# Performance work log

Hardware: AMD Instinct MI355X
Metric: run time of the kernel (lower is better)

Reference implementation:

```python
import jax, jax.numpy as jnp
import numpy as np

ALPHA = 0.1
DEPTH = 10

N_NODES = 100000
N_EDGES = 3200000
FEATS = 512
HIDDEN = 64
CLASSES = 32


def setup_inputs() -> dict:
    key = jax.random.key(0)
    k1, k2, k3, k4 = jax.random.split(key, 4)
    x = jax.random.normal(k1, (N_NODES, FEATS), dtype=jnp.float32)
    edges = jax.random.randint(k2, (2, N_EDGES), 0, N_NODES, dtype=jnp.int64)
    # Linear weights (stored as [in, out] so forward is x @ W + b)
    W1 = jax.random.normal(k3, (FEATS, HIDDEN), dtype=jnp.float32) * (1.0 / np.sqrt(FEATS))
    b1 = jnp.zeros((HIDDEN,), dtype=jnp.float32)
    W2 = jax.random.normal(k4, (HIDDEN, CLASSES), dtype=jnp.float32) * (1.0 / np.sqrt(HIDDEN))
    b2 = jnp.zeros((CLASSES,), dtype=jnp.float32)
    return {"x": x, "edges": edges, "W1": W1, "b1": b1, "W2": W2, "b2": b2}


def reference(x, edges, W1, b1, W2, b2):
    # Eval mode: all dropouts (feature + edge) are identity.
    n = x.shape[0]
    src, dst = edges[0], edges[1]

    # Symmetric normalization 1/sqrt(deg_src * deg_dst), degrees from in-edges.
    deg = jax.ops.segment_sum(jnp.ones_like(dst, dtype=x.dtype), dst, num_segments=n)
    deg = jnp.maximum(deg, 1.0)
    norm = jax.lax.rsqrt(deg[src] * deg[dst])  # [E]

    # MLP: feats -> hidden -> classes
    h = jax.nn.relu(x @ W1 + b1) @ W2 + b2  # [N, classes]
    h0 = h

    # APPNP propagation: x <- (1-alpha) * A_hat x + alpha * h0
    for _ in range(DEPTH):
        msg = h[src] * norm[:, None]                          # gather  [E, classes]
        agg = jax.ops.segment_sum(msg, dst, num_segments=n)   # scatter [N, classes]
        h = agg * (1.0 - ALPHA) + ALPHA * h0
    return h
```

## Files before the change

### kernel.cpp

```cpp
#include <hip/hip_runtime.h>

#define ALPHA_F 0.1f
#define DEPTH 10
#define FEATS 512
#define HID 64
#define CLS 32

__device__ __forceinline__ unsigned bf16rne(float f) {
  unsigned u = __float_as_uint(f);
  return (u + 0x7fffu + ((u >> 16) & 1u)) >> 16;
}

__global__ __launch_bounds__(256) void k_deg(const int* __restrict__ dst, int E, int N,
                                             unsigned* __restrict__ deg,
                                             unsigned* __restrict__ rank) {
  int i = blockIdx.x * 256 + threadIdx.x;
  if (i >= E) return;
  int d = dst[i];
  unsigned r = 0;
  if ((unsigned)d < (unsigned)N) r = atomicAdd(&deg[d], 1u);
  rank[i] = r;
}

__global__ __launch_bounds__(1024) void k_scan(const unsigned* __restrict__ deg, int N,
                                               unsigned* __restrict__ rowst) {
  __shared__ unsigned sums[1024];
  int t = threadIdx.x;
  int chunk = (N + 1023) >> 10;
  int beg = t * chunk;
  int end = min(beg + chunk, N);
  unsigned s = 0;
  for (int i = beg; i < end; ++i) s += deg[i];
  sums[t] = s;
  __syncthreads();
  for (int off = 1; off < 1024; off <<= 1) {
    unsigned v = (t >= off) ? sums[t - off] : 0u;
    __syncthreads();
    sums[t] += v;
    __syncthreads();
  }
  unsigned pre = (t == 0) ? 0u : sums[t - 1];
  for (int i = beg; i < end; ++i) { rowst[i] = pre; pre += deg[i]; }
  if (t == 1023) rowst[N] = pre;
}

__global__ __launch_bounds__(256) void k_fill(const int* __restrict__ src,
                                              const int* __restrict__ dst,
                                              const unsigned* __restrict__ rank,
                                              const unsigned* __restrict__ rowst,
                                              int E, int N,
                                              int* __restrict__ col) {
  int e = blockIdx.x * 256 + threadIdx.x;
  if (e >= E) return;
  int s = src[e];
  int d = dst[e];
  if ((unsigned)s >= (unsigned)N || (unsigned)d >= (unsigned)N) return;
  col[rowst[d] + rank[e]] = s;
}

__global__ __launch_bounds__(256) void k_mlp(const float* __restrict__ x,
                                             const float* __restrict__ W1,
                                             const float* __restrict__ b1,
                                             const float* __restrict__ W2,
                                             const float* __restrict__ b2,
                                             const unsigned* __restrict__ deg,
                                             float* __restrict__ h0,
                                             unsigned short* __restrict__ u0,
                                             float* __restrict__ rs, int N) {
  __shared__ float XHs[64 * 65];
  __shared__ float W2s[64 * 32];
  __shared__ float b1s[64];
  __shared__ float b2s[32];
  int t = threadIdx.x;
  int m0 = blockIdx.x * 64;

  for (int i = t; i < 64 * 32; i += 256) W2s[i] = W2[i];
  if (t < 64) b1s[t] = b1[t];
  if (t < 32) b2s[t] = b2[t];

  int c = t & 31;
  int h = t >> 5;
  float acc[8][2];
#pragma unroll
  for (int i = 0; i < 8; ++i) { acc[i][0] = 0.f; acc[i][1] = 0.f; }

  for (int k0 = 0; k0 < FEATS; k0 += 64) {
    __syncthreads();
#pragma unroll
    for (int j = 0; j < 2; ++j) {
      int F = j * 256 + t;
      int r = F >> 3, q = F & 7;
      int row = m0 + r;
      float4 v = make_float4(0.f, 0.f, 0.f, 0.f);
      if (row < N) v = *(const float4*)(x + (size_t)row * FEATS + k0 + q * 8);
      *(float4*)(XHs + r * 64 + q * 8) = v;
      float4 v2 = make_float4(0.f, 0.f, 0.f, 0.f);
      if (row < N) v2 = *(const float4*)(x + (size_t)row * FEATS + k0 + q * 8 + 4);
      *(float4*)(XHs + r * 64 + q * 8 + 4) = v2;
    }
    __syncthreads();
    const float* W1p = W1 + (size_t)k0 * 64;
#pragma unroll
    for (int k4 = 0; k4 < 16; ++k4) {
      int k = k4 * 4;
      float4 xv[8];
#pragma unroll
      for (int i = 0; i < 8; ++i) xv[i] = *(const float4*)(XHs + (h * 8 + i) * 64 + k);
#pragma unroll
      for (int j = 0; j < 4; ++j) {
        float w0 = W1p[(k + j) * 64 + c];
        float w1 = W1p[(k + j) * 64 + c + 32];
#pragma unroll
        for (int i = 0; i < 8; ++i) {
          float xx = ((const float*)&xv[i])[j];
          acc[i][0] += xx * w0;
          acc[i][1] += xx * w1;
        }
      }
    }
  }
  __syncthreads();
#pragma unroll
  for (int i = 0; i < 8; ++i) {
    int r = h * 8 + i;
    float v0 = acc[i][0] + b1s[c];
    float v1 = acc[i][1] + b1s[c + 32];
    XHs[r * 65 + c] = v0 > 0.f ? v0 : 0.f;
    XHs[r * 65 + c + 32] = v1 > 0.f ? v1 : 0.f;
  }
  __syncthreads();
  int cc = t & 31;
#pragma unroll
  for (int i = 0; i < 8; ++i) {
    int r = h * 8 + i;
    float s = b2s[cc];
#pragma unroll
    for (int k = 0; k < 64; ++k) s += XHs[r * 65 + k] * W2s[k * 32 + cc];
    int row = m0 + r;
    if (row < N) {
      float dv = (float)deg[row];
      float rsv = rsqrtf(fmaxf(dv, 1.0f));
      h0[(size_t)row * CLS + cc] = s;
      u0[(size_t)row * CLS + cc] = (unsigned short)bf16rne(rsv * s);
      if (cc == 0) rs[row] = rsv;
    }
  }
}

template <bool LAST>
__global__ __launch_bounds__(256) void k_prop(const unsigned* __restrict__ u_in,
                                              const float* __restrict__ h0,
                                              const float* __restrict__ rs,
                                              const unsigned* __restrict__ rowst,
                                              const int* __restrict__ col,
                                              void* __restrict__ out, int N) {
  int t = blockIdx.x * 256 + threadIdx.x;
  int node = t >> 3;
  if (node >= N) return;
  int l = t & 7;
  unsigned beg = rowst[node];
  unsigned end = rowst[node + 1];
  const unsigned* up = u_in + l * 2;
  float a0 = 0.f, a1 = 0.f, a2 = 0.f, a3 = 0.f;
  float b0 = 0.f, b1v = 0.f, b2v = 0.f, b3 = 0.f;
  unsigned e = beg;
  for (; e + 8 <= end; e += 8) {
    int s0 = col[e + 0], s1 = col[e + 1], s2 = col[e + 2], s3 = col[e + 3];
    int s4 = col[e + 4], s5 = col[e + 5], s6 = col[e + 6], s7 = col[e + 7];
    uint2 q0 = *(const uint2*)(up + (size_t)s0 * 16);
    uint2 q1 = *(const uint2*)(up + (size_t)s1 * 16);
    uint2 q2 = *(const uint2*)(up + (size_t)s2 * 16);
    uint2 q3 = *(const uint2*)(up + (size_t)s3 * 16);
    uint2 q4 = *(const uint2*)(up + (size_t)s4 * 16);
    uint2 q5 = *(const uint2*)(up + (size_t)s5 * 16);
    uint2 q6 = *(const uint2*)(up + (size_t)s6 * 16);
    uint2 q7 = *(const uint2*)(up + (size_t)s7 * 16);
    a0 += __uint_as_float(q0.x << 16) + __uint_as_float(q1.x << 16);
    a1 += __uint_as_float(q0.x & 0xffff0000u) + __uint_as_float(q1.x & 0xffff0000u);
    a2 += __uint_as_float(q0.y << 16) + __uint_as_float(q1.y << 16);
    a3 += __uint_as_float(q0.y & 0xffff0000u) + __uint_as_float(q1.y & 0xffff0000u);
    b0 += __uint_as_float(q2.x << 16) + __uint_as_float(q3.x << 16);
    b1v += __uint_as_float(q2.x & 0xffff0000u) + __uint_as_float(q3.x & 0xffff0000u);
    b2v += __uint_as_float(q2.y << 16) + __uint_as_float(q3.y << 16);
    b3 += __uint_as_float(q2.y & 0xffff0000u) + __uint_as_float(q3.y & 0xffff0000u);
    a0 += __uint_as_float(q4.x << 16) + __uint_as_float(q5.x << 16);
    a1 += __uint_as_float(q4.x & 0xffff0000u) + __uint_as_float(q5.x & 0xffff0000u);
    a2 += __uint_as_float(q4.y << 16) + __uint_as_float(q5.y << 16);
    a3 += __uint_as_float(q4.y & 0xffff0000u) + __uint_as_float(q5.y & 0xffff0000u);
    b0 += __uint_as_float(q6.x << 16) + __uint_as_float(q7.x << 16);
    b1v += __uint_as_float(q6.x & 0xffff0000u) + __uint_as_float(q7.x & 0xffff0000u);
    b2v += __uint_as_float(q6.y << 16) + __uint_as_float(q7.y << 16);
    b3 += __uint_as_float(q6.y & 0xffff0000u) + __uint_as_float(q7.y & 0xffff0000u);
  }
  for (; e < end; ++e) {
    int s = col[e];
    uint2 q = *(const uint2*)(up + (size_t)s * 16);
    a0 += __uint_as_float(q.x << 16);
    a1 += __uint_as_float(q.x & 0xffff0000u);
    a2 += __uint_as_float(q.y << 16);
    a3 += __uint_as_float(q.y & 0xffff0000u);
  }
  a0 += b0; a1 += b1v; a2 += b2v; a3 += b3;
  float rsv = rs[node];
  float4 h0v = *(const float4*)(h0 + (size_t)node * CLS + l * 4);
  if (LAST) {
    float ca = ALPHA_F, cb = (1.0f - ALPHA_F) * rsv;
    float4 o = make_float4(ca * h0v.x + cb * a0, ca * h0v.y + cb * a1,
                           ca * h0v.z + cb * a2, ca * h0v.w + cb * a3);
    *(float4*)((float*)out + (size_t)node * CLS + l * 4) = o;
  } else {
    float ca = ALPHA_F * rsv, cb = (1.0f - ALPHA_F) * rsv * rsv;
    float o0 = ca * h0v.x + cb * a0, o1 = ca * h0v.y + cb * a1;
    float o2 = ca * h0v.z + cb * a2, o3 = ca * h0v.w + cb * a3;
    uint2 p;
    p.x = bf16rne(o0) | (bf16rne(o1) << 16);
    p.y = bf16rne(o2) | (bf16rne(o3) << 16);
    *(uint2*)((unsigned*)out + (size_t)node * 16 + l * 2) = p;
  }
}

extern "C" void kernel_launch(void* const* d_in, const int* in_sizes, int n_in,
                              void* d_out, int out_size, void* d_ws, size_t ws_size,
                              hipStream_t stream) {
  const float* x = (const float*)d_in[0];
  const int* edges = (const int*)d_in[1];
  const float* W1 = (const float*)d_in[2];
  const float* b1 = (const float*)d_in[3];
  const float* W2 = (const float*)d_in[4];
  const float* b2 = (const float*)d_in[5];
  int N = in_sizes[0] / FEATS;
  int E = in_sizes[1] / 2;
  const int* src = edges;
  const int* dst = edges + E;

  char* ws = (char*)d_ws;
  auto align64 = [](size_t v) { return (v + 63) & ~(size_t)63; };
  size_t o = 0;
  unsigned* deg = (unsigned*)(ws + o);   o = align64(o + (size_t)N * 4);
  unsigned* rowst = (unsigned*)(ws + o); o = align64(o + (size_t)(N + 1) * 4);
  float* rs = (float*)(ws + o);          o = align64(o + (size_t)N * 4);
  int* col = (int*)(ws + o);             o = align64(o + (size_t)E * 4);
  float* h0 = (float*)(ws + o);          o = align64(o + (size_t)N * CLS * 4);
  unsigned* uA = (unsigned*)(ws + o);    o = align64(o + (size_t)N * CLS * 2);
  unsigned* uB = (unsigned*)(ws + o);    o = align64(o + (size_t)N * CLS * 2);
  unsigned* rank = (unsigned*)h0;

  hipMemsetAsync(deg, 0, (size_t)N * 4, stream);
  k_deg<<<(E + 255) / 256, 256, 0, stream>>>(dst, E, N, deg, rank);
  k_scan<<<1, 1024, 0, stream>>>(deg, N, rowst);
  k_fill<<<(E + 255) / 256, 256, 0, stream>>>(src, dst, rank, rowst, E, N, col);
  k_mlp<<<(N + 63) / 64, 256, 0, stream>>>(x, W1, b1, W2, b2, deg, h0,
                                           (unsigned short*)uA, rs, N);

  float* outF = (float*)d_out;
  const unsigned* uin = uA;
  for (int it = 0; it < DEPTH - 1; ++it) {
    unsigned* uo = (it & 1) ? uA : uB;
    k_prop<false><<<((N * 8) + 255) / 256, 256, 0, stream>>>(uin, h0, rs, rowst, col, uo, N);
    uin = uo;
  }
  k_prop<true><<<((N * 8) + 255) / 256, 256, 0, stream>>>(uin, h0, rs, rowst, col, outF, N);
}
```

Baseline: 1.151 ms.

## Widen MLP tile to 128 rows and use 4 lanes per node in propagation

The MLP kernel now processes 128 rows per block with a 4x8 register tile per thread, loading W1 as float4 and padding the shared tile to stride 68. The point is more register reuse and fewer global W1 loads per FMA. The propagation kernel drops from 8 to 4 lanes per node, each gathering 16 bytes (8 bf16 features) per neighbor instead of 8. That halves the gather instruction count, at the cost of higher register pressure and less thread-level parallelism across the irregular edge lists.

```diff
diff --git a/kernel.cpp b/kernel.cpp
--- a/kernel.cpp
+++ b/kernel.cpp
@@ -10,6 +10,8 @@
   unsigned u = __float_as_uint(f);
   return (u + 0x7fffu + ((u >> 16) & 1u)) >> 16;
 }
+__device__ __forceinline__ float blo(unsigned q) { return __uint_as_float(q << 16); }
+__device__ __forceinline__ float bhi(unsigned q) { return __uint_as_float(q & 0xffff0000u); }
 
 __global__ __launch_bounds__(256) void k_deg(const int* __restrict__ dst, int E, int N,
                                              unsigned* __restrict__ deg,
@@ -67,36 +69,35 @@
                                              float* __restrict__ h0,
                                              unsigned short* __restrict__ u0,
                                              float* __restrict__ rs, int N) {
-  __shared__ float XHs[64 * 65];
+  __shared__ float XHs[128 * 68];
   __shared__ float W2s[64 * 32];
   __shared__ float b1s[64];
   __shared__ float b2s[32];
   int t = threadIdx.x;
-  int m0 = blockIdx.x * 64;
+  int m0 = blockIdx.x * 128;
 
   for (int i = t; i < 64 * 32; i += 256) W2s[i] = W2[i];
   if (t < 64) b1s[t] = b1[t];
   if (t < 32) b2s[t] = b2[t];
 
-  int c = t & 31;
-  int h = t >> 5;
-  float acc[8][2];
-#pragma unroll
-  for (int i = 0; i < 8; ++i) { acc[i][0] = 0.f; acc[i][1] = 0.f; }
+  int c4 = t & 15;
+  int hg = t >> 4;
+  float acc[8][4];
+#pragma unroll
+  for (int i = 0; i < 8; ++i)
+#pragma unroll
+    for (int m = 0; m < 4; ++m) acc[i][m] = 0.f;
 
   for (int k0 = 0; k0 < FEATS; k0 += 64) {
     __syncthreads();
 #pragma unroll
-    for (int j = 0; j < 2; ++j) {
+    for (int j = 0; j < 8; ++j) {
       int F = j * 256 + t;
-      int r = F >> 3, q = F & 7;
+      int r = F >> 4, q = F & 15;
       int row = m0 + r;
       float4 v = make_float4(0.f, 0.f, 0.f, 0.f);
-      if (row < N) v = *(const float4*)(x + (size_t)row * FEATS + k0 + q * 8);
-      *(float4*)(XHs + r * 64 + q * 8) = v;
-      float4 v2 = make_float4(0.f, 0.f, 0.f, 0.f);
-      if (row < N) v2 = *(const float4*)(x + (size_t)row * FEATS + k0 + q * 8 + 4);
-      *(float4*)(XHs + r * 64 + q * 8 + 4) = v2;
+      if (row < N) v = *(const float4*)(x + (size_t)row * FEATS + k0 + q * 4);
+      *(float4*)(XHs + r * 68 + q * 4) = v;
     }
     __syncthreads();
     const float* W1p = W1 + (size_t)k0 * 64;
@@ -105,16 +106,19 @@
       int k = k4 * 4;
       float4 xv[8];
 #pragma unroll
-      for (int i = 0; i < 8; ++i) xv[i] = *(const float4*)(XHs + (h * 8 + i) * 64 + k);
+      for (int i = 0; i < 8; ++i) xv[i] = *(const float4*)(XHs + (i * 16 + hg) * 68 + k);
+      float4 w[4];
+#pragma unroll
+      for (int j = 0; j < 4; ++j) w[j] = *(const float4*)(W1p + (size_t)(k + j) * 64 + c4 * 4);
 #pragma unroll
       for (int j = 0; j < 4; ++j) {
-        float w0 = W1p[(k + j) * 64 + c];
-        float w1 = W1p[(k + j) * 64 + c + 32];
 #pragma unroll
         for (int i = 0; i < 8; ++i) {
           float xx = ((const float*)&xv[i])[j];
-          acc[i][0] += xx * w0;
-          acc[i][1] += xx * w1;
+          acc[i][0] += xx * w[j].x;
+          acc[i][1] += xx * w[j].y;
+          acc[i][2] += xx * w[j].z;
+          acc[i][3] += xx * w[j].w;
         }
       }
     }
@@ -122,20 +126,22 @@
   __syncthreads();
 #pragma unroll
   for (int i = 0; i < 8; ++i) {
-    int r = h * 8 + i;
-    float v0 = acc[i][0] + b1s[c];
-    float v1 = acc[i][1] + b1s[c + 32];
-    XHs[r * 65 + c] = v0 > 0.f ? v0 : 0.f;
-    XHs[r * 65 + c + 32] = v1 > 0.f ? v1 : 0.f;
+    int r = i * 16 + hg;
+    float4 o;
+    o.x = fmaxf(acc[i][0] + b1s[c4 * 4 + 0], 0.f);
+    o.y = fmaxf(acc[i][1] + b1s[c4 * 4 + 1], 0.f);
+    o.z = fmaxf(acc[i][2] + b1s[c4 * 4 + 2], 0.f);
+    o.w = fmaxf(acc[i][3] + b1s[c4 * 4 + 3], 0.f);
+    *(float4*)(XHs + r * 68 + c4 * 4) = o;
   }
   __syncthreads();
-  int cc = t & 31;
-#pragma unroll
-  for (int i = 0; i < 8; ++i) {
-    int r = h * 8 + i;
+  int cc = t & 31, g = t >> 5;
+#pragma unroll
+  for (int i = 0; i < 16; ++i) {
+    int r = i * 8 + g;
     float s = b2s[cc];
 #pragma unroll
-    for (int k = 0; k < 64; ++k) s += XHs[r * 65 + k] * W2s[k * 32 + cc];
+    for (int k = 0; k < 64; ++k) s += XHs[r * 68 + k] * W2s[k * 32 + cc];
     int row = m0 + r;
     if (row < N) {
       float dv = (float)deg[row];
@@ -155,67 +161,75 @@
                                               const int* __restrict__ col,
                                               void* __restrict__ out, int N) {
   int t = blockIdx.x * 256 + threadIdx.x;
-  int node = t >> 3;
+  int node = t >> 2;
   if (node >= N) return;
-  int l = t & 7;
+  int l = t & 3;
   unsigned beg = rowst[node];
   unsigned end = rowst[node + 1];
-  const unsigned* up = u_in + l * 2;
-  float a0 = 0.f, a1 = 0.f, a2 = 0.f, a3 = 0.f;
-  float b0 = 0.f, b1v = 0.f, b2v = 0.f, b3 = 0.f;
+  const uint4* up = (const uint4*)u_in + l;
+  float a[8], b[8];
+#pragma unroll
+  for (int j = 0; j < 8; ++j) { a[j] = 0.f; b[j] = 0.f; }
   unsigned e = beg;
   for (; e + 8 <= end; e += 8) {
     int s0 = col[e + 0], s1 = col[e + 1], s2 = col[e + 2], s3 = col[e + 3];
     int s4 = col[e + 4], s5 = col[e + 5], s6 = col[e + 6], s7 = col[e + 7];
-    uint2 q0 = *(const uint2*)(up + (size_t)s0 * 16);
-    uint2 q1 = *(const uint2*)(up + (size_t)s1 * 16);
-    uint2 q2 = *(const uint2*)(up + (size_t)s2 * 16);
-    uint2 q3 = *(const uint2*)(up + (size_t)s3 * 16);
-    uint2 q4 = *(const uint2*)(up + (size_t)s4 * 16);
-    uint2 q5 = *(const uint2*)(up + (size_t)s5 * 16);
-    uint2 q6 = *(const uint2*)(up + (size_t)s6 * 16);
-    uint2 q7 = *(const uint2*)(up + (size_t)s7 * 16);
-    a0 += __uint_as_float(q0.x << 16) + __uint_as_float(q1.x << 16);
-    a1 += __uint_as_float(q0.x & 0xffff0000u) + __uint_as_float(q1.x & 0xffff0000u);
-    a2 += __uint_as_float(q0.y << 16) + __uint_as_float(q1.y << 16);
-    a3 += __uint_as_float(q0.y & 0xffff0000u) + __uint_as_float(q1.y & 0xffff0000u);
-    b0 += __uint_as_float(q2.x << 16) + __uint_as_float(q3.x << 16);
-    b1v += __uint_as_float(q2.x & 0xffff0000u) + __uint_as_float(q3.x & 0xffff0000u);
-    b2v += __uint_as_float(q2.y << 16) + __uint_as_float(q3.y << 16);
-    b3 += __uint_as_float(q2.y & 0xffff0000u) + __uint_as_float(q3.y & 0xffff0000u);
-    a0 += __uint_as_float(q4.x << 16) + __uint_as_float(q5.x << 16);
-    a1 += __uint_as_float(q4.x & 0xffff0000u) + __uint_as_float(q5.x & 0xffff0000u);
-    a2 += __uint_as_float(q4.y << 16) + __uint_as_float(q5.y << 16);
-    a3 += __uint_as_float(q4.y & 0xffff0000u) + __uint_as_float(q5.y & 0xffff0000u);
-    b0 += __uint_as_float(q6.x << 16) + __uint_as_float(q7.x << 16);
-    b1v += __uint_as_float(q6.x & 0xffff0000u) + __uint_as_float(q7.x & 0xffff0000u);
-    b2v += __uint_as_float(q6.y << 16) + __uint_as_float(q7.y << 16);
-    b3 += __uint_as_float(q6.y & 0xffff0000u) + __uint_as_float(q7.y & 0xffff0000u);
+    uint4 q0 = up[(size_t)s0 * 4];
+    uint4 q1 = up[(size_t)s1 * 4];
+    uint4 q2 = up[(size_t)s2 * 4];
+    uint4 q3 = up[(size_t)s3 * 4];
+    uint4 q4 = up[(size_t)s4 * 4];
+    uint4 q5 = up[(size_t)s5 * 4];
+    uint4 q6 = up[(size_t)s6 * 4];
+    uint4 q7 = up[(size_t)s7 * 4];
+    a[0] += blo(q0.x); a[1] += bhi(q0.x); a[2] += blo(q0.y); a[3] += bhi(q0.y);
+    a[4] += blo(q0.z); a[5] += bhi(q0.z); a[6] += blo(q0.w); a[7] += bhi(q0.w);
+    b[0] += blo(q1.x); b[1] += bhi(q1.x); b[2] += blo(q1.y); b[3] += bhi(q1.y);
+    b[4] += blo(q1.z); b[5] += bhi(q1.z); b[6] += blo(q1.w); b[7] += bhi(q1.w);
+    a[0] += blo(q2.x); a[1] += bhi(q2.x); a[2] += blo(q2.y); a[3] += bhi(q2.y);
+    a[4] += blo(q2.z); a[5] += bhi(q2.z); a[6] += blo(q2.w); a[7] += bhi(q2.w);
+    b[0] += blo(q3.x); b[1] += bhi(q3.x); b[2] += blo(q3.y); b[3] += bhi(q3.y);
+    b[4] += blo(q3.z); b[5] += bhi(q3.z); b[6] += blo(q3.w); b[7] += bhi(q3.w);
+    a[0] += blo(q4.x); a[1] += bhi(q4.x); a[2] += blo(q4.y); a[3] += bhi(q4.y);
+    a[4] += blo(q4.z); a[5] += bhi(q4.z); a[6] += blo(q4.w); a[7] += bhi(q4.w);
+    b[0] += blo(q5.x); b[1] += bhi(q5.x); b[2] += blo(q5.y); b[3] += bhi(q5.y);
+    b[4] += blo(q5.z); b[5] += bhi(q5.z); b[6] += blo(q5.w); b[7] += bhi(q5.w);
+    a[0] += blo(q6.x); a[1] += bhi(q6.x); a[2] += blo(q6.y); a[3] += bhi(q6.y);
+    a[4] += blo(q6.z); a[5] += bhi(q6.z); a[6] += blo(q6.w); a[7] += bhi(q6.w);
+    b[0] += blo(q7.x); b[1] += bhi(q7.x); b[2] += blo(q7.y); b[3] += bhi(q7.y);
+    b[4] += blo(q7.z); b[5] += bhi(q7.z); b[6] += blo(q7.w); b[7] += bhi(q7.w);
   }
   for (; e < end; ++e) {
     int s = col[e];
-    uint2 q = *(const uint2*)(up + (size_t)s * 16);
-    a0 += __uint_as_float(q.x << 16);
-    a1 += __uint_as_float(q.x & 0xffff0000u);
-    a2 += __uint_as_float(q.y << 16);
-    a3 += __uint_as_float(q.y & 0xffff0000u);
-  }
-  a0 += b0; a1 += b1v; a2 += b2v; a3 += b3;
+    uint4 q = up[(size_t)s * 4];
+    a[0] += blo(q.x); a[1] += bhi(q.x); a[2] += blo(q.y); a[3] += bhi(q.y);
+    a[4] += blo(q.z); a[5] += bhi(q.z); a[6] += blo(q.w); a[7] += bhi(q.w);
+  }
+#pragma unroll
+  for (int j = 0; j < 8; ++j) a[j] += b[j];
   float rsv = rs[node];
-  float4 h0v = *(const float4*)(h0 + (size_t)node * CLS + l * 4);
+  const float* h0p = h0 + (size_t)node * CLS + l * 8;
+  float4 h0a = *(const float4*)(h0p);
+  float4 h0b = *(const float4*)(h0p + 4);
   if (LAST) {
     float ca = ALPHA_F, cb = (1.0f - ALPHA_F) * rsv;
-    float4 o = make_float4(ca * h0v.x + cb * a0, ca * h0v.y + cb * a1,
-                           ca * h0v.z + cb * a2, ca * h0v.w + cb * a3);
-    *(float4*)((float*)out + (size_t)node * CLS + l * 4) = o;
+    float* op = (float*)out + (size_t)node * CLS + l * 8;
+    *(float4*)(op) = make_float4(ca * h0a.x + cb * a[0], ca * h0a.y + cb * a[1],
+                                 ca * h0a.z + cb * a[2], ca * h0a.w + cb * a[3]);
+    *(float4*)(op + 4) = make_float4(ca * h0b.x + cb * a[4], ca * h0b.y + cb * a[5],
+                                     ca * h0b.z + cb * a[6], ca * h0b.w + cb * a[7]);
   } else {
     float ca = ALPHA_F * rsv, cb = (1.0f - ALPHA_F) * rsv * rsv;
-    float o0 = ca * h0v.x + cb * a0, o1 = ca * h0v.y + cb * a1;
-    float o2 = ca * h0v.z + cb * a2, o3 = ca * h0v.w + cb * a3;
-    uint2 p;
+    float o0 = ca * h0a.x + cb * a[0], o1 = ca * h0a.y + cb * a[1];
+    float o2 = ca * h0a.z + cb * a[2], o3 = ca * h0a.w + cb * a[3];
+    float o4 = ca * h0b.x + cb * a[4], o5 = ca * h0b.y + cb * a[5];
+    float o6 = ca * h0b.z + cb * a[6], o7 = ca * h0b.w + cb * a[7];
+    uint4 p;
     p.x = bf16rne(o0) | (bf16rne(o1) << 16);
     p.y = bf16rne(o2) | (bf16rne(o3) << 16);
-    *(uint2*)((unsigned*)out + (size_t)node * 16 + l * 2) = p;
+    p.z = bf16rne(o4) | (bf16rne(o5) << 16);
+    p.w = bf16rne(o6) | (bf16rne(o7) << 16);
+    *((uint4*)out + (size_t)node * 4 + l) = p;
   }
 }
 
@@ -249,15 +263,15 @@
   k_deg<<<(E + 255) / 256, 256, 0, stream>>>(dst, E, N, deg, rank);
   k_scan<<<1, 1024, 0, stream>>>(deg, N, rowst);
   k_fill<<<(E + 255) / 256, 256, 0, stream>>>(src, dst, rank, rowst, E, N, col);
-  k_mlp<<<(N + 63) / 64, 256, 0, stream>>>(x, W1, b1, W2, b2, deg, h0,
-                                           (unsigned short*)uA, rs, N);
+  k_mlp<<<(N + 127) / 128, 256, 0, stream>>>(x, W1, b1, W2, b2, deg, h0,
+                                             (unsigned short*)uA, rs, N);
 
   float* outF = (float*)d_out;
   const unsigned* uin = uA;
   for (int it = 0; it < DEPTH - 1; ++it) {
     unsigned* uo = (it & 1) ? uA : uB;
-    k_prop<false><<<((N * 8) + 255) / 256, 256, 0, stream>>>(uin, h0, rs, rowst, col, uo, N);
+    k_prop<false><<<((N * 4) + 255) / 256, 256, 0, stream>>>(uin, h0, rs, rowst, col, uo, N);
     uin = uo;
   }
-  k_prop<true><<<((N * 8) + 255) / 256, 256, 0, stream>>>(uin, h0, rs, rowst, col, outF, N);
-}
+  k_prop<true><<<((N * 4) + 255) / 256, 256, 0, stream>>>(uin, h0, rs, rowst, col, outF, N);
+}
```

After: 1.244 ms. 1.08x slower.

## Pad CSR rows to multiples of 16 with dummy node and widen per-lane gathers

Applied to the files above, without the earlier changes.

Builds a padded CSR in which each row's length is rounded up to a multiple of 16 and the padding slots point to a zeroed dummy node N. The propagation kernel can then drop its remainder loop, read column indices as uint4 vectors and do 16 gathers per iteration. Each node now gets 4 lanes with 16-byte loads instead of 8 lanes with 8-byte loads. h0 is also stored as bf16 to halve that read. The cost is extra padded edge work (up to 15 per node, on average degree 32), an extra col-init kernel, and lower precision in h0.

```diff
diff --git a/kernel.cpp b/kernel.cpp
--- a/kernel.cpp
+++ b/kernel.cpp
@@ -3,13 +3,14 @@
 #define ALPHA_F 0.1f
 #define DEPTH 10
 #define FEATS 512
-#define HID 64
 #define CLS 32
 
 __device__ __forceinline__ unsigned bf16rne(float f) {
   unsigned u = __float_as_uint(f);
   return (u + 0x7fffu + ((u >> 16) & 1u)) >> 16;
 }
+__device__ __forceinline__ float blo(unsigned q) { return __uint_as_float(q << 16); }
+__device__ __forceinline__ float bhi(unsigned q) { return __uint_as_float(q & 0xffff0000u); }
 
 __global__ __launch_bounds__(256) void k_deg(const int* __restrict__ dst, int E, int N,
                                              unsigned* __restrict__ deg,
@@ -22,15 +23,15 @@
   rank[i] = r;
 }
 
-__global__ __launch_bounds__(1024) void k_scan(const unsigned* __restrict__ deg, int N,
-                                               unsigned* __restrict__ rowst) {
+__global__ __launch_bounds__(1024) void k_scanp(const unsigned* __restrict__ deg, int N,
+                                                unsigned* __restrict__ rowst2) {
   __shared__ unsigned sums[1024];
   int t = threadIdx.x;
   int chunk = (N + 1023) >> 10;
   int beg = t * chunk;
   int end = min(beg + chunk, N);
   unsigned s = 0;
-  for (int i = beg; i < end; ++i) s += deg[i];
+  for (int i = beg; i < end; ++i) s += (deg[i] + 15u) & ~15u;
   sums[t] = s;
   __syncthreads();
   for (int off = 1; off < 1024; off <<= 1) {
@@ -40,22 +41,27 @@
     __syncthreads();
   }
   unsigned pre = (t == 0) ? 0u : sums[t - 1];
-  for (int i = beg; i < end; ++i) { rowst[i] = pre; pre += deg[i]; }
-  if (t == 1023) rowst[N] = pre;
+  for (int i = beg; i < end; ++i) { rowst2[i] = pre; pre += (deg[i] + 15u) & ~15u; }
+  if (t == 1023) rowst2[N] = pre;
+}
+
+__global__ __launch_bounds__(256) void k_colinit(unsigned* __restrict__ col2, int cap, int N) {
+  int i = blockIdx.x * 256 + threadIdx.x;
+  if (i < cap) col2[i] = (unsigned)N;
 }
 
 __global__ __launch_bounds__(256) void k_fill(const int* __restrict__ src,
                                               const int* __restrict__ dst,
                                               const unsigned* __restrict__ rank,
-                                              const unsigned* __restrict__ rowst,
+                                              const unsigned* __restrict__ rowst2,
                                               int E, int N,
-                                              int* __restrict__ col) {
+                                              unsigned* __restrict__ col2) {
   int e = blockIdx.x * 256 + threadIdx.x;
   if (e >= E) return;
   int s = src[e];
   int d = dst[e];
   if ((unsigned)s >= (unsigned)N || (unsigned)d >= (unsigned)N) return;
-  col[rowst[d] + rank[e]] = s;
+  col2[rowst2[d] + rank[e]] = (unsigned)s;
 }
 
 __global__ __launch_bounds__(256) void k_mlp(const float* __restrict__ x,
@@ -64,7 +70,7 @@
                                              const float* __restrict__ W2,
                                              const float* __restrict__ b2,
                                              const unsigned* __restrict__ deg,
-                                             float* __restrict__ h0,
+                                             unsigned short* __restrict__ h0b,
                                              unsigned short* __restrict__ u0,
                                              float* __restrict__ rs, int N) {
   __shared__ float XHs[64 * 65];
@@ -140,7 +146,7 @@
     if (row < N) {
       float dv = (float)deg[row];
       float rsv = rsqrtf(fmaxf(dv, 1.0f));
-      h0[(size_t)row * CLS + cc] = s;
+      h0b[(size_t)row * CLS + cc] = (unsigned short)bf16rne(s);
       u0[(size_t)row * CLS + cc] = (unsigned short)bf16rne(rsv * s);
       if (cc == 0) rs[row] = rsv;
     }
@@ -149,73 +155,73 @@
 
 template <bool LAST>
 __global__ __launch_bounds__(256) void k_prop(const unsigned* __restrict__ u_in,
-                                              const float* __restrict__ h0,
+                                              const unsigned short* __restrict__ h0b,
                                               const float* __restrict__ rs,
-                                              const unsigned* __restrict__ rowst,
-                                              const int* __restrict__ col,
+                                              const unsigned* __restrict__ rowst2,
+                                              const unsigned* __restrict__ col2,
                                               void* __restrict__ out, int N) {
   int t = blockIdx.x * 256 + threadIdx.x;
-  int node = t >> 3;
-  if (node >= N) return;
-  int l = t & 7;
-  unsigned beg = rowst[node];
-  unsigned end = rowst[node + 1];
-  const unsigned* up = u_in + l * 2;
-  float a0 = 0.f, a1 = 0.f, a2 = 0.f, a3 = 0.f;
-  float b0 = 0.f, b1v = 0.f, b2v = 0.f, b3 = 0.f;
-  unsigned e = beg;
-  for (; e + 8 <= end; e += 8) {
-    int s0 = col[e + 0], s1 = col[e + 1], s2 = col[e + 2], s3 = col[e + 3];
-    int s4 = col[e + 4], s5 = col[e + 5], s6 = col[e + 6], s7 = col[e + 7];
-    uint2 q0 = *(const uint2*)(up + (size_t)s0 * 16);
-    uint2 q1 = *(const uint2*)(up + (size_t)s1 * 16);
-    uint2 q2 = *(const uint2*)(up + (size_t)s2 * 16);
-    uint2 q3 = *(const uint2*)(up + (size_t)s3 * 16);
-    uint2 q4 = *(const uint2*)(up + (size_t)s4 * 16);
-    uint2 q5 = *(const uint2*)(up + (size_t)s5 * 16);
-    uint2 q6 = *(const uint2*)(up + (size_t)s6 * 16);
-    uint2 q7 = *(const uint2*)(up + (size_t)s7 * 16);
-    a0 += __uint_as_float(q0.x << 16) + __uint_as_float(q1.x << 16);
-    a1 += __uint_as_float(q0.x & 0xffff0000u) + __uint_as_float(q1.x & 0xffff0000u);
-    a2 += __uint_as_float(q0.y << 16) + __uint_as_float(q1.y << 16);
-    a3 += __uint_as_float(q0.y & 0xffff0000u) + __uint_as_float(q1.y & 0xffff0000u);
-    b0 += __uint_as_float(q2.x << 16) + __uint_as_float(q3.x << 16);
-    b1v += __uint_as_float(q2.x & 0xffff0000u) + __uint_as_float(q3.x & 0xffff0000u);
-    b2v += __uint_as_float(q2.y << 16) + __uint_as_float(q3.y << 16);
-    b3 += __uint_as_float(q2.y & 0xffff0000u) + __uint_as_float(q3.y & 0xffff0000u);
-    a0 += __uint_as_float(q4.x << 16) + __uint_as_float(q5.x << 16);
-    a1 += __uint_as_float(q4.x & 0xffff0000u) + __uint_as_float(q5.x & 0xffff0000u);
-    a2 += __uint_as_float(q4.y << 16) + __uint_as_float(q5.y << 16);
-    a3 += __uint_as_float(q4.y & 0xffff0000u) + __uint_as_float(q5.y & 0xffff0000u);
-    b0 += __uint_as_float(q6.x << 16) + __uint_as_float(q7.x << 16);
-    b1v += __uint_as_float(q6.x & 0xffff0000u) + __uint_as_float(q7.x & 0xffff0000u);
-    b2v += __uint_as_float(q6.y << 16) + __uint_as_float(q7.y << 16);
-    b3 += __uint_as_float(q6.y & 0xffff0000u) + __uint_as_float(q7.y & 0xffff0000u);
-  }
-  for (; e < end; ++e) {
-    int s = col[e];
-    uint2 q = *(const uint2*)(up + (size_t)s * 16);
-    a0 += __uint_as_float(q.x << 16);
-    a1 += __uint_as_float(q.x & 0xffff0000u);
-    a2 += __uint_as_float(q.y << 16);
-    a3 += __uint_as_float(q.y & 0xffff0000u);
-  }
-  a0 += b0; a1 += b1v; a2 += b2v; a3 += b3;
-  float rsv = rs[node];
-  float4 h0v = *(const float4*)(h0 + (size_t)node * CLS + l * 4);
+  int g = t >> 2;
+  if (g >= N) return;
+  int l = t & 3;
+  unsigned beg = rowst2[g];
+  unsigned end = rowst2[g + 1];
+  const uint4* up = (const uint4*)u_in + l;
+  const uint4* colv = (const uint4*)col2;
+  float a[8];
+#pragma unroll
+  for (int j = 0; j < 8; ++j) a[j] = 0.f;
+  for (unsigned e = beg; e < end; e += 16) {
+    unsigned e4 = e >> 2;
+    uint4 c0 = colv[e4 + 0];
+    uint4 c1 = colv[e4 + 1];
+    uint4 c2 = colv[e4 + 2];
+    uint4 c3 = colv[e4 + 3];
+    uint4 q0 = up[(size_t)c0.x * 4];
+    uint4 q1 = up[(size_t)c0.y * 4];
+    uint4 q2 = up[(size_t)c0.z * 4];
+    uint4 q3 = up[(size_t)c0.w * 4];
+    uint4 q4 = up[(size_t)c1.x * 4];
+    uint4 q5 = up[(size_t)c1.y * 4];
+    uint4 q6 = up[(size_t)c1.z * 4];
+    uint4 q7 = up[(size_t)c1.w * 4];
+    uint4 q8 = up[(size_t)c2.x * 4];
+    uint4 q9 = up[(size_t)c2.y * 4];
+    uint4 qa = up[(size_t)c2.z * 4];
+    uint4 qb = up[(size_t)c2.w * 4];
+    uint4 qc = up[(size_t)c3.x * 4];
+    uint4 qd = up[(size_t)c3.y * 4];
+    uint4 qe = up[(size_t)c3.z * 4];
+    uint4 qf = up[(size_t)c3.w * 4];
+#define ACC(q) \
+    a[0] += blo(q.x); a[1] += bhi(q.x); a[2] += blo(q.y); a[3] += bhi(q.y); \
+    a[4] += blo(q.z); a[5] += bhi(q.z); a[6] += blo(q.w); a[7] += bhi(q.w);
+    ACC(q0) ACC(q1) ACC(q2) ACC(q3) ACC(q4) ACC(q5) ACC(q6) ACC(q7)
+    ACC(q8) ACC(q9) ACC(qa) ACC(qb) ACC(qc) ACC(qd) ACC(qe) ACC(qf)
+#undef ACC
+  }
+  float rsv = rs[g];
+  uint4 hq = *((const uint4*)h0b + (size_t)g * 4 + l);
+  float h0v[8] = { blo(hq.x), bhi(hq.x), blo(hq.y), bhi(hq.y),
+                   blo(hq.z), bhi(hq.z), blo(hq.w), bhi(hq.w) };
   if (LAST) {
     float ca = ALPHA_F, cb = (1.0f - ALPHA_F) * rsv;
-    float4 o = make_float4(ca * h0v.x + cb * a0, ca * h0v.y + cb * a1,
-                           ca * h0v.z + cb * a2, ca * h0v.w + cb * a3);
-    *(float4*)((float*)out + (size_t)node * CLS + l * 4) = o;
+    float* op = (float*)out + (size_t)g * CLS + l * 8;
+    *(float4*)(op) = make_float4(ca * h0v[0] + cb * a[0], ca * h0v[1] + cb * a[1],
+                                 ca * h0v[2] + cb * a[2], ca * h0v[3] + cb * a[3]);
+    *(float4*)(op + 4) = make_float4(ca * h0v[4] + cb * a[4], ca * h0v[5] + cb * a[5],
+                                     ca * h0v[6] + cb * a[6], ca * h0v[7] + cb * a[7]);
   } else {
     float ca = ALPHA_F * rsv, cb = (1.0f - ALPHA_F) * rsv * rsv;
-    float o0 = ca * h0v.x + cb * a0, o1 = ca * h0v.y + cb * a1;
-    float o2 = ca * h0v.z + cb * a2, o3 = ca * h0v.w + cb * a3;
-    uint2 p;
-    p.x = bf16rne(o0) | (bf16rne(o1) << 16);
-    p.y = bf16rne(o2) | (bf16rne(o3) << 16);
-    *(uint2*)((unsigned*)out + (size_t)node * 16 + l * 2) = p;
+    float o[8];
+#pragma unroll
+    for (int j = 0; j < 8; ++j) o[j] = ca * h0v[j] + cb * a[j];
+    uint4 p;
+    p.x = bf16rne(o[0]) | (bf16rne(o[1]) << 16);
+    p.y = bf16rne(o[2]) | (bf16rne(o[3]) << 16);
+    p.z = bf16rne(o[4]) | (bf16rne(o[5]) << 16);
+    p.w = bf16rne(o[6]) | (bf16rne(o[7]) << 16);
+    *((uint4*)out + (size_t)g * 4 + l) = p;
   }
 }
 
@@ -232,32 +238,38 @@
   int E = in_sizes[1] / 2;
   const int* src = edges;
   const int* dst = edges + E;
+  int cap = E + 16 * N;
 
   char* ws = (char*)d_ws;
   auto align64 = [](size_t v) { return (v + 63) & ~(size_t)63; };
   size_t o = 0;
-  unsigned* deg = (unsigned*)(ws + o);   o = align64(o + (size_t)N * 4);
-  unsigned* rowst = (unsigned*)(ws + o); o = align64(o + (size_t)(N + 1) * 4);
-  float* rs = (float*)(ws + o);          o = align64(o + (size_t)N * 4);
-  int* col = (int*)(ws + o);             o = align64(o + (size_t)E * 4);
-  float* h0 = (float*)(ws + o);          o = align64(o + (size_t)N * CLS * 4);
-  unsigned* uA = (unsigned*)(ws + o);    o = align64(o + (size_t)N * CLS * 2);
-  unsigned* uB = (unsigned*)(ws + o);    o = align64(o + (size_t)N * CLS * 2);
-  unsigned* rank = (unsigned*)h0;
+  unsigned* deg = (unsigned*)(ws + o);    o = align64(o + (size_t)N * 4);
+  unsigned* rowst2 = (unsigned*)(ws + o); o = align64(o + (size_t)(N + 1) * 4);
+  float* rs = (float*)(ws + o);           o = align64(o + (size_t)N * 4);
+  unsigned* rank = (unsigned*)(ws + o);   o = align64(o + (size_t)E * 4);
+  unsigned* col2 = (unsigned*)(ws + o);   o = align64(o + (size_t)cap * 4);
+  unsigned short* h0b = (unsigned short*)(ws + o); o = align64(o + (size_t)N * CLS * 2);
+  unsigned* uA = (unsigned*)(ws + o);     o = align64(o + (size_t)(N + 1) * CLS * 2);
+  unsigned* uB = (unsigned*)(ws + o);     o = align64(o + (size_t)(N + 1) * CLS * 2);
 
   hipMemsetAsync(deg, 0, (size_t)N * 4, stream);
+  hipMemsetAsync(uA + (size_t)N * 16, 0, 64, stream);
+  hipMemsetAsync(uB + (size_t)N * 16, 0, 64, stream);
   k_deg<<<(E + 255) / 256, 256, 0, stream>>>(dst, E, N, deg, rank);
-  k_scan<<<1, 1024, 0, stream>>>(deg, N, rowst);
-  k_fill<<<(E + 255) / 256, 256, 0, stream>>>(src, dst, rank, rowst, E, N, col);
-  k_mlp<<<(N + 63) / 64, 256, 0, stream>>>(x, W1, b1, W2, b2, deg, h0,
+  k_scanp<<<1, 1024, 0, stream>>>(deg, N, rowst2);
+  k_colinit<<<(cap + 255) / 256, 256, 0, stream>>>(col2, cap, N);
+  k_fill<<<(E + 255) / 256, 256, 0, stream>>>(src, dst, rank, rowst2, E, N, col2);
+  k_mlp<<<(N + 63) / 64, 256, 0, stream>>>(x, W1, b1, W2, b2, deg, h0b,
                                            (unsigned short*)uA, rs, N);
 
   float* outF = (float*)d_out;
   const unsigned* uin = uA;
   for (int it = 0; it < DEPTH - 1; ++it) {
     unsigned* uo = (it & 1) ? uA : uB;
-    k_prop<false><<<((N * 8) + 255) / 256, 256, 0, stream>>>(uin, h0, rs, rowst, col, uo, N);
+    k_prop<false><<<((N * 4) + 255) / 256, 256, 0, stream>>>(uin, h0b, rs, rowst2, col2,
+                                                             uo, N);
     uin = uo;
   }
-  k_prop<true><<<((N * 8) + 255) / 256, 256, 0, stream>>>(uin, h0, rs, rowst, col, outF, N);
-}
+  k_prop<true><<<((N * 4) + 255) / 256, 256, 0, stream>>>(uin, h0b, rs, rowst2, col2,
+                                                          outF, N);
+}
```

New measurement: 1.120 ms. 1.03x faster.
